# Optimization experiments

Hardware: AMD Instinct MI355X
Metric: run time of the kernel (lower is better)

## Reference

```python
import jax, jax.numpy as jnp
import numpy as np

N_NODES = 100000
N_EDGES = 1600000
IN_DIM = 128      # 1 (degree) + 127 (raw feat)
HID = 128
N_GRAPHS = 100


def setup_inputs() -> dict:
    key = jax.random.key(0)
    ks = jax.random.split(key, 16)
    feat = jax.random.normal(ks[0], (N_NODES, IN_DIM - 1), dtype=jnp.float32)
    src = jax.random.randint(ks[1], (N_EDGES,), 0, N_NODES, dtype=jnp.int32)
    dst = jax.random.randint(ks[2], (N_EDGES,), 0, N_NODES, dtype=jnp.int32)
    graph_ids = jnp.sort(jax.random.randint(ks[3], (N_NODES,), 0, N_GRAPHS, dtype=jnp.int32))
    s = 1.0 / np.sqrt(IN_DIM)
    W0 = jax.random.uniform(ks[4], (HID, IN_DIM), jnp.float32, -s, s)
    b0 = jax.random.uniform(ks[5], (HID,), jnp.float32, -s, s)
    s = 1.0 / np.sqrt(HID)
    W1 = jax.random.uniform(ks[6], (HID, HID), jnp.float32, -s, s)
    b1 = jax.random.uniform(ks[7], (HID,), jnp.float32, -s, s)
    W2 = jax.random.uniform(ks[8], (HID, HID), jnp.float32, -s, s)
    b2 = jax.random.uniform(ks[9], (HID,), jnp.float32, -s, s)
    Wc1 = jax.random.uniform(ks[10], (HID, HID), jnp.float32, -s, s)
    bc1 = jax.random.uniform(ks[11], (HID,), jnp.float32, -s, s)
    Wc2 = jax.random.uniform(ks[12], (1, HID), jnp.float32, -s, s)
    bc2 = jax.random.uniform(ks[13], (1,), jnp.float32, -s, s)
    return {"feat": feat, "src": src, "dst": dst, "graph_ids": graph_ids,
            "num_graphs": N_GRAPHS,
            "W0": W0, "b0": b0, "W1": W1, "b1": b1, "W2": W2, "b2": b2,
            "Wc1": Wc1, "bc1": bc1, "Wc2": Wc2, "bc2": bc2}


def _gcn_layer(h, src, dst, deg, W, b):
    # mean over in-neighbor messages; zero-in-degree nodes keep old h (DGL reduce never fires)
    n = h.shape[0]
    summed = jax.ops.segment_sum(h[src], dst, num_segments=n)  # [N, d]
    mean = summed / jnp.maximum(deg, 1.0)[:, None]
    agg = jnp.where((deg > 0)[:, None], mean, h)
    return jax.nn.relu(agg @ W.T + b)


def reference(feat, src, dst, graph_ids, num_graphs,
              W0, b0, W1, b1, W2, b2, Wc1, bc1, Wc2, bc2):
    n = feat.shape[0]
    deg = jax.ops.segment_sum(jnp.ones(src.shape[0], jnp.float32), dst, num_segments=n)  # in-degrees
    h = jnp.concatenate([deg[:, None], feat], axis=-1)  # [N, IN_DIM]
    for W, b in ((W0, b0), (W1, b1), (W2, b2)):
        h = _gcn_layer(h, src, dst, deg, W, b)
    # dgl.mean_nodes: per-graph mean of node features
    counts = jax.ops.segment_sum(jnp.ones(n, jnp.float32), graph_ids, num_segments=num_graphs)
    hg = jax.ops.segment_sum(h, graph_ids, num_segments=num_graphs) / jnp.maximum(counts, 1.0)[:, None]
    # faithful: classify1 applied twice, no activation (F.relu was passed as bias flag)
    hg = hg @ Wc1.T + bc1
    hg = hg @ Wc1.T + bc1
    hg = hg @ Wc2.T + bc2
    return hg  # [num_graphs, 1]
```

## Files before the change

### kernel.cpp

```cpp
#include <hip/hip_runtime.h>
#include <hip/hip_bf16.h>

#define HID 128
#define NRAW 127
#define BSH 8
#define BNODES 256


typedef __attribute__((ext_vector_type(8))) short short8;
typedef __attribute__((ext_vector_type(4))) float floatx4;
typedef __attribute__((ext_vector_type(2))) float floatx2;

__device__ inline unsigned pack_bf2(float x, float y) {
    unsigned bx = __float_as_uint(x);
    unsigned by = __float_as_uint(y);
    bx += 0x7fffu + ((bx >> 16) & 1u);
    by += 0x7fffu + ((by >> 16) & 1u);
    return (bx >> 16) | (by & 0xffff0000u);
}
__device__ inline float bf_lo(unsigned u) { return __uint_as_float(u << 16); }
__device__ inline float bf_hi(unsigned u) { return __uint_as_float(u & 0xffff0000u); }


__global__ void init_kernel(const float* __restrict__ W0, const float* __restrict__ W1,
                            const float* __restrict__ W2, const float* __restrict__ Wc1,
                            unsigned* __restrict__ O0, unsigned* __restrict__ O1,
                            unsigned* __restrict__ O2, float* __restrict__ Wc1p,
                            int* __restrict__ gbucket, float* __restrict__ hg,
                            float* __restrict__ counts,
                            unsigned* __restrict__ h8a, unsigned* __restrict__ h8b,
                            int G, int N) {
    int id = blockIdx.x * blockDim.x + threadIdx.x;
    if (id < 512) gbucket[id] = 0;
    if (id < G * HID) hg[id] = 0.f;
    if (id < G) counts[id] = 0.f;
    if (id < 32) {
        h8a[(size_t)N * 32 + id] = 0u;
        h8b[(size_t)N * 32 + id] = 0u;
    }
    if (id < 16384) {
        int t = id >> 7, p = id & 127;
        Wc1p[id] = Wc1[t * 128 + ((p & 7) * 16 + (p >> 3))];
    }
    if (id < 3 * 8192) {
        int sel = id >> 13, l = id & 8191;
        const float* W = sel == 0 ? W0 : (sel == 1 ? W1 : W2);
        unsigned* O = sel == 0 ? O0 : (sel == 1 ? O1 : O2);
        int o = l >> 6, pp = (l & 63) * 2;
        int k0 = (pp & 7) * 16 + (pp >> 3);
        int k1 = ((pp + 1) & 7) * 16 + ((pp + 1) >> 3);
        O[l] = pack_bf2(W[o * 128 + k0], W[o * 128 + k1]);
    }
}


__global__ __launch_bounds__(256) void bucket_count_kernel(const int* __restrict__ dst,
                                                           int* __restrict__ gbucket,
                                                           int E, int NB) {
    __shared__ int hist[512];
    int t = threadIdx.x;
    for (int b = t; b < NB; b += 256) hist[b] = 0;
    __syncthreads();
    int base = blockIdx.x * 4096;
    #pragma unroll
    for (int j = 0; j < 16; ++j) {
        int e = base + j * 256 + t;
        if (e < E) atomicAdd(&hist[dst[e] >> BSH], 1);
    }
    __syncthreads();
    for (int b = t; b < NB; b += 256) {
        int v = hist[b];
        if (v) atomicAdd(&gbucket[b], v);
    }
}

__global__ void bucket_scan_kernel(const int* __restrict__ gbucket, int* __restrict__ bstart,
                                   int* __restrict__ gcur, int NB, int E) {
    __shared__ int sm[512];
    int t = threadIdx.x;
    int v = (t < NB) ? gbucket[t] : 0;
    sm[t] = v;
    __syncthreads();
    for (int off = 1; off < 512; off <<= 1) {
        int add = (t >= off) ? sm[t - off] : 0;
        __syncthreads();
        sm[t] += add;
        __syncthreads();
    }
    if (t < NB) {
        int ex = sm[t] - v;
        bstart[t] = ex;
        gcur[t] = ex;
    }
    if (t == 0) bstart[NB] = E;
}

__global__ __launch_bounds__(256) void bucket_scatter_kernel(const int* __restrict__ src,
                                                             const int* __restrict__ dst,
                                                             int* __restrict__ gcur,
                                                             unsigned* __restrict__ staging,
                                                             int E, int NB) {
    __shared__ int hist[512];
    __shared__ int base[512];
    int t = threadIdx.x;
    for (int b = t; b < NB; b += 256) hist[b] = 0;
    __syncthreads();
    int s[16], d[16], r[16];
    int e0 = blockIdx.x * 4096;
    #pragma unroll
    for (int j = 0; j < 16; ++j) {
        int e = e0 + j * 256 + t;
        if (e < E) {
            s[j] = src[e];
            d[j] = dst[e];
            r[j] = atomicAdd(&hist[d[j] >> BSH], 1);
        } else d[j] = -1;
    }
    __syncthreads();
    for (int b = t; b < NB; b += 256) {
        int v = hist[b];
        base[b] = v ? atomicAdd(&gcur[b], v) : 0;
    }
    __syncthreads();
    #pragma unroll
    for (int j = 0; j < 16; ++j) {
        if (d[j] >= 0) {
            int b = d[j] >> BSH;
            staging[base[b] + r[j]] = ((unsigned)s[j] << 8) | ((unsigned)d[j] & 255u);
        }
    }
}

__global__ __launch_bounds__(256) void csr_build_kernel(const unsigned* __restrict__ staging,
                                                        const int* __restrict__ bstart,
                                                        int* __restrict__ rp, int* __restrict__ csr,
                                                        float* __restrict__ degf,
                                                        int N, int E, int NB) {
    __shared__ int hist[256];
    __shared__ int sm[256];
    __shared__ int excl[256];
    __shared__ int cnt[256];
    int t = threadIdx.x;
    int b = blockIdx.x;
    int nbase = b << BSH;
    int s0 = bstart[b], e1 = bstart[b + 1];
    hist[t] = 0;
    __syncthreads();
    for (int i = s0 + t; i < e1; i += 256) {
        unsigned p = staging[i];
        atomicAdd(&hist[p & (BNODES - 1)], 1);
    }
    __syncthreads();
    int h = hist[t];
    sm[t] = h;
    __syncthreads();
    for (int off = 1; off < 256; off <<= 1) {
        int add = (t >= off) ? sm[t - off] : 0;
        __syncthreads();
        sm[t] += add;
        __syncthreads();
    }
    excl[t] = sm[t] - h;
    cnt[t] = 0;
    int n = nbase + t;
    if (n < N) {
        rp[n] = s0 + (sm[t] - h);
        degf[n] = (float)h;
    }
    if (b == NB - 1 && t == 0) {
        rp[N] = E;
        degf[N] = 0.f;
    }
    __syncthreads();
    for (int i = s0 + t; i < e1; i += 256) {
        unsigned p = staging[i];
        int dl = p & (BNODES - 1);
        int pos = s0 + excl[dl] + atomicAdd(&cnt[dl], 1);
        csr[pos] = (int)(p >> 8);
    }
}


__global__ __launch_bounds__(256) void build_h0_kernel(const float* __restrict__ feat,
                                                       unsigned* __restrict__ h8, int N) {
    __shared__ float lf[8 * NRAW];
    int t = threadIdx.x;
    int n0 = blockIdx.x * 8;
    int nrows = min(8, N - n0);
    int total = nrows * NRAW;
    for (int j = t; j < total; j += 256) lf[j] = feat[(size_t)n0 * NRAW + j];
    __syncthreads();
    int n = t >> 5, c = t & 31;
    if (n < nrows) {
        const float* fr = lf + n * NRAW;
        int base = c >> 1, hb = (c & 1) * 4;
        float f[4];
        #pragma unroll
        for (int j = 0; j < 4; ++j) {
            int l = (hb + j) * 16 + base;
            f[j] = (l == 0) ? 0.f : fr[l - 1];
        }
        unsigned w = __builtin_amdgcn_cvt_pk_fp8_f32(f[0], f[1], 0, false);
        w = __builtin_amdgcn_cvt_pk_fp8_f32(f[2], f[3], w, true);
        h8[(size_t)(n0 + n) * 32 + c] = w;
    }
}


__global__ __launch_bounds__(256) void gcn_fused_kernel(const unsigned* __restrict__ h8,
                                                        unsigned* __restrict__ out8,
                                                        unsigned* __restrict__ outb,
                                                        const unsigned* __restrict__ Wb,
                                                        const float* __restrict__ bias,
                                                        const int* __restrict__ rp,
                                                        const int* __restrict__ csr,
                                                        const float* __restrict__ degf,
                                                        int col0fix, int N) {
    __shared__ unsigned Al[16 * 64];
    __shared__ unsigned Cs[16 * 64];
    int t = threadIdx.x;
    int wv = t >> 6, lane = t & 63;
    int s = lane >> 4;
    int c = lane & 15;
    int n0 = blockIdx.x * 16;
    const char* hbase = (const char*)h8;
    unsigned cOff = (unsigned)c * 8u;

    for (int nn = 0; nn < 4; ++nn) {
        int g = wv * 4 + nn;
        int i = n0 + g;
        if (i >= N) break;
        int start = rp[i], end = rp[i + 1];
        int deg = end - start;
        floatx2 a0 = {0.f, 0.f}, a1 = {0.f, 0.f}, a2 = {0.f, 0.f}, a3 = {0.f, 0.f};
        float dsum = 0.f;

        if (deg > 0) {
            int q = start + s;
            int idx = N;
            if (q < end) idx = csr[q];
            for (int p = start; p < end; p += 4) {
                uint2 v = *(const uint2*)(hbase + (((unsigned)idx << 7) + cOff));
                float dg = 0.f;
                if (col0fix && c == 0) dg = degf[idx];
                int q2 = p + 4 + s;
                int idxN = N;
                if (q2 < end) idxN = csr[q2];
                a0 += __builtin_amdgcn_cvt_pk_f32_fp8(v.x, false);
                a1 += __builtin_amdgcn_cvt_pk_f32_fp8(v.x, true);
                a2 += __builtin_amdgcn_cvt_pk_f32_fp8(v.y, false);
                a3 += __builtin_amdgcn_cvt_pk_f32_fp8(v.y, true);
                if (col0fix && c == 0) dsum += dg;
                idx = idxN;
            }
            a0[0] += __shfl_xor(a0[0], 16); a0[1] += __shfl_xor(a0[1], 16);
            a1[0] += __shfl_xor(a1[0], 16); a1[1] += __shfl_xor(a1[1], 16);
            a2[0] += __shfl_xor(a2[0], 16); a2[1] += __shfl_xor(a2[1], 16);
            a3[0] += __shfl_xor(a3[0], 16); a3[1] += __shfl_xor(a3[1], 16);
            a0[0] += __shfl_xor(a0[0], 32); a0[1] += __shfl_xor(a0[1], 32);
            a1[0] += __shfl_xor(a1[0], 32); a1[1] += __shfl_xor(a1[1], 32);
            a2[0] += __shfl_xor(a2[0], 32); a2[1] += __shfl_xor(a2[1], 32);
            a3[0] += __shfl_xor(a3[0], 32); a3[1] += __shfl_xor(a3[1], 32);
            if (col0fix) {
                dsum += __shfl_xor(dsum, 16);
                dsum += __shfl_xor(dsum, 32);
            }
        }

        float f0, f1, f2, f3, f4, f5, f6, f7;
        if (deg > 0) {
            if (col0fix && c == 0) a0[0] = dsum;
            float inv = 1.f / (float)deg;
            f0 = a0[0] * inv; f1 = a0[1] * inv;
            f2 = a1[0] * inv; f3 = a1[1] * inv;
            f4 = a2[0] * inv; f5 = a2[1] * inv;
            f6 = a3[0] * inv; f7 = a3[1] * inv;
        } else {
            uint2 v = *(const uint2*)(hbase + (((unsigned)i << 7) + cOff));
            floatx2 l0 = __builtin_amdgcn_cvt_pk_f32_fp8(v.x, false);
            floatx2 h0 = __builtin_amdgcn_cvt_pk_f32_fp8(v.x, true);
            floatx2 l1 = __builtin_amdgcn_cvt_pk_f32_fp8(v.y, false);
            floatx2 h1 = __builtin_amdgcn_cvt_pk_f32_fp8(v.y, true);
            f0 = l0[0]; f1 = l0[1]; f2 = h0[0]; f3 = h0[1];
            f4 = l1[0]; f5 = l1[1]; f6 = h1[0]; f7 = h1[1];
        }
        if (s == 0) {
            uint4 r;
            r.x = pack_bf2(f0, f1);
            r.y = pack_bf2(f2, f3);
            r.z = pack_bf2(f4, f5);
            r.w = pack_bf2(f6, f7);
            *(uint4*)&Al[(g * 16 + (c ^ (g & 7))) * 4] = r;
        }
    }
    __syncthreads();

    {
        int m = lane & 15, q = lane >> 4;
        floatx4 acc0 = (floatx4)(0.f), acc1 = (floatx4)(0.f);
        #pragma unroll
        for (int kt = 0; kt < 4; ++kt) {
            short8 af = *(const short8*)&Al[(m * 16 + ((kt * 4 + q) ^ (m & 7))) * 4];
            short8 b0 = *(const short8*)&Wb[((2 * wv) * 16 + m) * 64 + kt * 16 + q * 4];
            short8 b1 = *(const short8*)&Wb[((2 * wv + 1) * 16 + m) * 64 + kt * 16 + q * 4];
            acc0 = __builtin_amdgcn_mfma_f32_16x16x32_bf16(af, b0, acc0, 0, 0, 0);
            acc1 = __builtin_amdgcn_mfma_f32_16x16x32_bf16(af, b1, acc1, 0, 0, 0);
        }
        float bv0 = bias[(2 * wv) * 16 + m];
        float bv1 = bias[(2 * wv + 1) * 16 + m];
        #pragma unroll
        for (int r4 = 0; r4 < 4; ++r4) {
            int row = q * 4 + r4;
            float v0 = fmaxf(acc0[r4] + bv0, 0.f);
            float v1 = fmaxf(acc1[r4] + bv1, 0.f);
            if (out8) {
                unsigned pk = __builtin_amdgcn_cvt_pk_fp8_f32(v0, v1, 0, false);
                *(unsigned short*)((char*)Cs + row * 128 + m * 8 + 2 * wv) = (unsigned short)pk;
            } else {
                Cs[row * 64 + m * 4 + wv] = pack_bf2(v0, v1);
            }
        }
    }
    __syncthreads();

    {
        int row = t >> 4, cc = t & 15;
        int n = n0 + row;
        if (n < N) {
            if (out8)
                ((uint2*)out8)[(size_t)n * 16 + cc] =
                    *(const uint2*)((const char*)Cs + row * 128 + cc * 8);
            else
                ((uint4*)outb)[(size_t)n * 16 + cc] = *(const uint4*)&Cs[row * 64 + cc * 4];
        }
    }
}


__global__ __launch_bounds__(256) void pool_kernel(const unsigned* __restrict__ h,
                                                   const int* __restrict__ gid,
                                                   float* __restrict__ hg,
                                                   float* __restrict__ counts, int N) {
    int c = threadIdx.x & 63;
    int q = threadIdx.x >> 6;
    int n0 = blockIdx.x * 64;
    int nend = min(n0 + 64, N);
    float ax = 0.f, ay = 0.f, cnt = 0.f;
    int cur = -1;
    for (int n = n0 + q; n < nend; n += 4) {
        int g = gid[n];
        if (g != cur) {
            if (cur >= 0) {
                atomicAdd(&hg[cur * HID + 2 * c], ax);
                atomicAdd(&hg[cur * HID + 2 * c + 1], ay);
                if (c == 0) atomicAdd(&counts[cur], cnt);
            }
            ax = ay = cnt = 0.f;
            cur = g;
        }
        unsigned v = h[(size_t)n * 64 + c];
        ax += bf_lo(v); ay += bf_hi(v);
        cnt += 1.f;
    }
    if (cur >= 0) {
        atomicAdd(&hg[cur * HID + 2 * c], ax);
        atomicAdd(&hg[cur * HID + 2 * c + 1], ay);
        if (c == 0) atomicAdd(&counts[cur], cnt);
    }
}


__global__ __launch_bounds__(128) void cls_fused_kernel(const float* __restrict__ hg,
                                                        const float* __restrict__ counts,
                                                        const float* __restrict__ Wc1p,
                                                        const float* __restrict__ Wc1,
                                                        const float* __restrict__ bc1,
                                                        const float* __restrict__ Wc2,
                                                        const float* __restrict__ bc2,
                                                        float* __restrict__ out, int G) {
    __shared__ float x[128];
    __shared__ float y[128];
    __shared__ float red[128];
    int g = blockIdx.x, t = threadIdx.x;
    float inv = 1.f / fmaxf(counts[g], 1.f);
    x[t] = hg[g * HID + t] * inv;
    __syncthreads();
    const float4* wp4 = (const float4*)(Wc1p + t * HID);
    float s = 0.f;
    #pragma unroll
    for (int k4 = 0; k4 < 32; ++k4) {
        float4 w = wp4[k4];
        s += x[k4 * 4] * w.x + x[k4 * 4 + 1] * w.y + x[k4 * 4 + 2] * w.z + x[k4 * 4 + 3] * w.w;
    }
    y[t] = s + bc1[t];
    __syncthreads();
    const float4* w4 = (const float4*)(Wc1 + t * HID);
    float s2 = 0.f;
    #pragma unroll
    for (int k4 = 0; k4 < 32; ++k4) {
        float4 w = w4[k4];
        s2 += y[k4 * 4] * w.x + y[k4 * 4 + 1] * w.y + y[k4 * 4 + 2] * w.z + y[k4 * 4 + 3] * w.w;
    }
    red[t] = (s2 + bc1[t]) * Wc2[t];
    __syncthreads();
    if (t < 64) {
        float r = red[t] + red[t + 64];
        #pragma unroll
        for (int off = 32; off > 0; off >>= 1) r += __shfl_down(r, off);
        if (t == 0) out[g] = r + bc2[0];
    }
}


extern "C" void kernel_launch(void* const* d_in, const int* in_sizes, int n_in,
                              void* d_out, int out_size, void* d_ws, size_t ws_size,
                              hipStream_t stream) {
    const float* feat = (const float*)d_in[0];
    const int* src    = (const int*)d_in[1];
    const int* dst    = (const int*)d_in[2];
    const int* gid    = (const int*)d_in[3];
    const float* W0  = (const float*)d_in[5];
    const float* b0  = (const float*)d_in[6];
    const float* W1  = (const float*)d_in[7];
    const float* b1  = (const float*)d_in[8];
    const float* W2  = (const float*)d_in[9];
    const float* b2  = (const float*)d_in[10];
    const float* Wc1 = (const float*)d_in[11];
    const float* bc1 = (const float*)d_in[12];
    const float* Wc2 = (const float*)d_in[13];
    const float* bc2 = (const float*)d_in[14];

    const int N = in_sizes[3];
    const int E = in_sizes[1];
    const int G = out_size;
    const int NB = (N + BNODES - 1) >> BSH;

    char* ws = (char*)d_ws;
    size_t off = 0;
    auto alloc = [&](size_t bytes) { void* p = ws + off; off += (bytes + 255) & ~size_t(255); return p; };
    unsigned* h8a    = (unsigned*)alloc((size_t)(N + 1) * 32 * 4);
    unsigned* h8b    = (unsigned*)alloc((size_t)(N + 1) * 32 * 4);
    unsigned* hB     = (unsigned*)alloc((size_t)N * 64 * 4);
    float* degf      = (float*)alloc((size_t)(N + 1) * 4);
    unsigned* staging = (unsigned*)alloc((size_t)E * 4);
    int* csr         = (int*)alloc((size_t)(E + 64) * 4);
    int* rp          = (int*)alloc((size_t)(N + 1) * 4);
    int* gbucket     = (int*)alloc(512 * 4);
    int* bstart      = (int*)alloc(513 * 4);
    int* gcur        = (int*)alloc(512 * 4);
    unsigned* Wb0    = (unsigned*)alloc(8192 * 4);
    unsigned* Wb1    = (unsigned*)alloc(8192 * 4);
    unsigned* Wb2    = (unsigned*)alloc(8192 * 4);
    float* Wc1p      = (float*)alloc(16384 * 4);
    float* hg        = (float*)alloc((size_t)G * HID * 4);
    float* counts    = (float*)alloc((size_t)G * 4);

    init_kernel<<<96, 256, 0, stream>>>(W0, W1, W2, Wc1, Wb0, Wb1, Wb2, Wc1p,
                                        gbucket, hg, counts, h8a, h8b, G, N);

    int gE = (E + 4095) / 4096;
    bucket_count_kernel<<<gE, 256, 0, stream>>>(dst, gbucket, E, NB);
    bucket_scan_kernel<<<1, 512, 0, stream>>>(gbucket, bstart, gcur, NB, E);
    bucket_scatter_kernel<<<gE, 256, 0, stream>>>(src, dst, gcur, staging, E, NB);
    csr_build_kernel<<<NB, 256, 0, stream>>>(staging, bstart, rp, csr, degf, N, E, NB);

    build_h0_kernel<<<(N + 7) / 8, 256, 0, stream>>>(feat, h8a, N);

    int layer_grid = (N + 15) / 16;
    gcn_fused_kernel<<<layer_grid, 256, 0, stream>>>(h8a, h8b, nullptr, Wb0, b0, rp, csr, degf, 1, N);
    gcn_fused_kernel<<<layer_grid, 256, 0, stream>>>(h8b, h8a, nullptr, Wb1, b1, rp, csr, degf, 0, N);
    gcn_fused_kernel<<<layer_grid, 256, 0, stream>>>(h8a, nullptr, hB, Wb2, b2, rp, csr, degf, 0, N);

    pool_kernel<<<(N + 63) / 64, 256, 0, stream>>>(hB, gid, hg, counts, N);

    cls_fused_kernel<<<G, 128, 0, stream>>>(hg, counts, Wc1p, Wc1, bc1, Wc2, bc2,
                                            (float*)d_out, G);
}
```

Baseline: 421.8 us.

## Restructure GCN gather: 8 lanes per node, staged CSR indices in LDS, 32-node tiles

```diff
diff --git a/kernel.cpp b/kernel.cpp
--- a/kernel.cpp
+++ b/kernel.cpp
@@ -5,6 +5,7 @@
 #define NRAW 127
 #define BSH 8
 #define BNODES 256
+#define EW 2048
 
 
 typedef __attribute__((ext_vector_type(8))) short short8;
@@ -207,133 +208,160 @@
 }
 
 
-__global__ __launch_bounds__(256) void gcn_fused_kernel(const unsigned* __restrict__ h8,
-                                                        unsigned* __restrict__ out8,
-                                                        unsigned* __restrict__ outb,
-                                                        const unsigned* __restrict__ Wb,
-                                                        const float* __restrict__ bias,
-                                                        const int* __restrict__ rp,
-                                                        const int* __restrict__ csr,
-                                                        const float* __restrict__ degf,
-                                                        int col0fix, int N) {
-    __shared__ unsigned Al[16 * 64];
-    __shared__ unsigned Cs[16 * 64];
+__global__ __launch_bounds__(256, 4) void gcn_fused_kernel(const unsigned* __restrict__ h8,
+                                                           unsigned* __restrict__ out8,
+                                                           unsigned* __restrict__ outb,
+                                                           const unsigned* __restrict__ Wb,
+                                                           const float* __restrict__ bias,
+                                                           const int* __restrict__ rp,
+                                                           const int* __restrict__ csr,
+                                                           const float* __restrict__ degf,
+                                                           int col0fix, int N) {
+    __shared__ unsigned Al[32 * 64];
+    __shared__ unsigned CsS[32 * 64];
+    int* sIdx = (int*)CsS;
     int t = threadIdx.x;
     int wv = t >> 6, lane = t & 63;
-    int s = lane >> 4;
-    int c = lane & 15;
-    int n0 = blockIdx.x * 16;
+    int grp = lane >> 3;
+    int cc4 = lane & 7;
+    int n0 = blockIdx.x * 32;
+    int g32 = wv * 8 + grp;
+    int i = n0 + g32;
     const char* hbase = (const char*)h8;
-    unsigned cOff = (unsigned)c * 8u;
-
-    for (int nn = 0; nn < 4; ++nn) {
-        int g = wv * 4 + nn;
-        int i = n0 + g;
-        if (i >= N) break;
-        int start = rp[i], end = rp[i + 1];
-        int deg = end - start;
-        floatx2 a0 = {0.f, 0.f}, a1 = {0.f, 0.f}, a2 = {0.f, 0.f}, a3 = {0.f, 0.f};
-        float dsum = 0.f;
-
-        if (deg > 0) {
-            int q = start + s;
-            int idx = N;
-            if (q < end) idx = csr[q];
-            for (int p = start; p < end; p += 4) {
-                uint2 v = *(const uint2*)(hbase + (((unsigned)idx << 7) + cOff));
-                float dg = 0.f;
-                if (col0fix && c == 0) dg = degf[idx];
-                int q2 = p + 4 + s;
-                int idxN = N;
-                if (q2 < end) idxN = csr[q2];
-                a0 += __builtin_amdgcn_cvt_pk_f32_fp8(v.x, false);
-                a1 += __builtin_amdgcn_cvt_pk_f32_fp8(v.x, true);
-                a2 += __builtin_amdgcn_cvt_pk_f32_fp8(v.y, false);
-                a3 += __builtin_amdgcn_cvt_pk_f32_fp8(v.y, true);
-                if (col0fix && c == 0) dsum += dg;
-                idx = idxN;
-            }
-            a0[0] += __shfl_xor(a0[0], 16); a0[1] += __shfl_xor(a0[1], 16);
-            a1[0] += __shfl_xor(a1[0], 16); a1[1] += __shfl_xor(a1[1], 16);
-            a2[0] += __shfl_xor(a2[0], 16); a2[1] += __shfl_xor(a2[1], 16);
-            a3[0] += __shfl_xor(a3[0], 16); a3[1] += __shfl_xor(a3[1], 16);
-            a0[0] += __shfl_xor(a0[0], 32); a0[1] += __shfl_xor(a0[1], 32);
-            a1[0] += __shfl_xor(a1[0], 32); a1[1] += __shfl_xor(a1[1], 32);
-            a2[0] += __shfl_xor(a2[0], 32); a2[1] += __shfl_xor(a2[1], 32);
-            a3[0] += __shfl_xor(a3[0], 32); a3[1] += __shfl_xor(a3[1], 32);
-            if (col0fix) {
-                dsum += __shfl_xor(dsum, 16);
-                dsum += __shfl_xor(dsum, 32);
-            }
-        }
-
-        float f0, f1, f2, f3, f4, f5, f6, f7;
-        if (deg > 0) {
-            if (col0fix && c == 0) a0[0] = dsum;
-            float inv = 1.f / (float)deg;
-            f0 = a0[0] * inv; f1 = a0[1] * inv;
-            f2 = a1[0] * inv; f3 = a1[1] * inv;
-            f4 = a2[0] * inv; f5 = a2[1] * inv;
-            f6 = a3[0] * inv; f7 = a3[1] * inv;
+    unsigned c16 = (unsigned)cc4 * 16u;
+
+    int start = 0, end = 0;
+    if (i < N) { start = rp[i]; end = rp[i + 1]; }
+    int deg = end - start;
+    int nEnd = min(n0 + 32, N);
+    int s0 = rp[n0];
+    int e1 = rp[nEnd];
+
+    floatx2 a0 = {0.f, 0.f}, a1 = {0.f, 0.f}, a2 = {0.f, 0.f}, a3 = {0.f, 0.f};
+    floatx2 a4 = {0.f, 0.f}, a5 = {0.f, 0.f}, a6 = {0.f, 0.f}, a7 = {0.f, 0.f};
+    float dsum = 0.f;
+
+    #define GATH4(ii) (*(const uint4*)(hbase + (((unsigned)(ii) << 7) + c16)))
+    #define ACC4(vv) do { \
+        a0 += __builtin_amdgcn_cvt_pk_f32_fp8((vv).x, false); \
+        a1 += __builtin_amdgcn_cvt_pk_f32_fp8((vv).x, true);  \
+        a2 += __builtin_amdgcn_cvt_pk_f32_fp8((vv).y, false); \
+        a3 += __builtin_amdgcn_cvt_pk_f32_fp8((vv).y, true);  \
+        a4 += __builtin_amdgcn_cvt_pk_f32_fp8((vv).z, false); \
+        a5 += __builtin_amdgcn_cvt_pk_f32_fp8((vv).z, true);  \
+        a6 += __builtin_amdgcn_cvt_pk_f32_fp8((vv).w, false); \
+        a7 += __builtin_amdgcn_cvt_pk_f32_fp8((vv).w, true);  \
+    } while (0)
+
+    for (int w0 = s0; w0 < e1; w0 += EW) {
+        if (w0 > s0) __syncthreads();
+        int wcnt = min(EW, e1 - w0);
+        for (int j = t; j < wcnt; j += 256) sIdx[j] = csr[w0 + j];
+        __syncthreads();
+        int p  = max(start, w0) - w0;
+        int pe = min(end, w0 + wcnt) - w0;
+        for (; p + 4 <= pe; p += 4) {
+            int iA = sIdx[p], iB = sIdx[p + 1], iC = sIdx[p + 2], iD = sIdx[p + 3];
+            uint4 vA = GATH4(iA), vB = GATH4(iB), vC = GATH4(iC), vD = GATH4(iD);
+            if (col0fix && cc4 == 0)
+                dsum += degf[iA] + degf[iB] + degf[iC] + degf[iD];
+            ACC4(vA); ACC4(vB); ACC4(vC); ACC4(vD);
+        }
+        for (; p + 2 <= pe; p += 2) {
+            int iA = sIdx[p], iB = sIdx[p + 1];
+            uint4 vA = GATH4(iA), vB = GATH4(iB);
+            if (col0fix && cc4 == 0) dsum += degf[iA] + degf[iB];
+            ACC4(vA); ACC4(vB);
+        }
+        for (; p < pe; ++p) {
+            int iA = sIdx[p];
+            uint4 vA = GATH4(iA);
+            if (col0fix && cc4 == 0) dsum += degf[iA];
+            ACC4(vA);
+        }
+    }
+
+    if (i < N) {
+        float inv;
+        if (deg == 0) {
+            uint4 v = GATH4(i);
+            ACC4(v);
+            inv = 1.f;
         } else {
-            uint2 v = *(const uint2*)(hbase + (((unsigned)i << 7) + cOff));
-            floatx2 l0 = __builtin_amdgcn_cvt_pk_f32_fp8(v.x, false);
-            floatx2 h0 = __builtin_amdgcn_cvt_pk_f32_fp8(v.x, true);
-            floatx2 l1 = __builtin_amdgcn_cvt_pk_f32_fp8(v.y, false);
-            floatx2 h1 = __builtin_amdgcn_cvt_pk_f32_fp8(v.y, true);
-            f0 = l0[0]; f1 = l0[1]; f2 = h0[0]; f3 = h0[1];
-            f4 = l1[0]; f5 = l1[1]; f6 = h1[0]; f7 = h1[1];
-        }
-        if (s == 0) {
-            uint4 r;
-            r.x = pack_bf2(f0, f1);
-            r.y = pack_bf2(f2, f3);
-            r.z = pack_bf2(f4, f5);
-            r.w = pack_bf2(f6, f7);
-            *(uint4*)&Al[(g * 16 + (c ^ (g & 7))) * 4] = r;
-        }
+            if (col0fix && cc4 == 0) a0[0] = dsum;
+            inv = 1.f / (float)deg;
+        }
+        uint4 r0, r1;
+        r0.x = pack_bf2(a0[0] * inv, a0[1] * inv);
+        r0.y = pack_bf2(a1[0] * inv, a1[1] * inv);
+        r0.z = pack_bf2(a2[0] * inv, a2[1] * inv);
+        r0.w = pack_bf2(a3[0] * inv, a3[1] * inv);
+        r1.x = pack_bf2(a4[0] * inv, a4[1] * inv);
+        r1.y = pack_bf2(a5[0] * inv, a5[1] * inv);
+        r1.z = pack_bf2(a6[0] * inv, a6[1] * inv);
+        r1.w = pack_bf2(a7[0] * inv, a7[1] * inv);
+        int gr0 = 2 * cc4, gr1 = 2 * cc4 + 1;
+        *(uint4*)&Al[(g32 * 16 + (gr0 ^ (g32 & 7))) * 4] = r0;
+        *(uint4*)&Al[(g32 * 16 + (gr1 ^ (g32 & 7))) * 4] = r1;
     }
     __syncthreads();
 
     {
+        int rh = wv & 1, cq = wv >> 1;
         int m = lane & 15, q = lane >> 4;
+        int r = rh * 16 + m;
         floatx4 acc0 = (floatx4)(0.f), acc1 = (floatx4)(0.f);
+        floatx4 acc2 = (floatx4)(0.f), acc3 = (floatx4)(0.f);
         #pragma unroll
         for (int kt = 0; kt < 4; ++kt) {
-            short8 af = *(const short8*)&Al[(m * 16 + ((kt * 4 + q) ^ (m & 7))) * 4];
-            short8 b0 = *(const short8*)&Wb[((2 * wv) * 16 + m) * 64 + kt * 16 + q * 4];
-            short8 b1 = *(const short8*)&Wb[((2 * wv + 1) * 16 + m) * 64 + kt * 16 + q * 4];
+            short8 af = *(const short8*)&Al[(r * 16 + ((kt * 4 + q) ^ (m & 7))) * 4];
+            short8 b0 = *(const short8*)&Wb[((cq * 4 + 0) * 16 + m) * 64 + kt * 16 + q * 4];
+            short8 b1 = *(const short8*)&Wb[((cq * 4 + 1) * 16 + m) * 64 + kt * 16 + q * 4];
+            short8 b2 = *(const short8*)&Wb[((cq * 4 + 2) * 16 + m) * 64 + kt * 16 + q * 4];
+            short8 b3 = *(const short8*)&Wb[((cq * 4 + 3) * 16 + m) * 64 + kt * 16 + q * 4];
             acc0 = __builtin_amdgcn_mfma_f32_16x16x32_bf16(af, b0, acc0, 0, 0, 0);
             acc1 = __builtin_amdgcn_mfma_f32_16x16x32_bf16(af, b1, acc1, 0, 0, 0);
-        }
-        float bv0 = bias[(2 * wv) * 16 + m];
-        float bv1 = bias[(2 * wv + 1) * 16 + m];
+            acc2 = __builtin_amdgcn_mfma_f32_16x16x32_bf16(af, b2, acc2, 0, 0, 0);
+            acc3 = __builtin_amdgcn_mfma_f32_16x16x32_bf16(af, b3, acc3, 0, 0, 0);
+        }
+        float bv0 = bias[(cq * 4 + 0) * 16 + m];
+        float bv1 = bias[(cq * 4 + 1) * 16 + m];
+        float bv2 = bias[(cq * 4 + 2) * 16 + m];
+        float bv3 = bias[(cq * 4 + 3) * 16 + m];
         #pragma unroll
         for (int r4 = 0; r4 < 4; ++r4) {
-            int row = q * 4 + r4;
+            int row = rh * 16 + q * 4 + r4;
             float v0 = fmaxf(acc0[r4] + bv0, 0.f);
             float v1 = fmaxf(acc1[r4] + bv1, 0.f);
+            float v2 = fmaxf(acc2[r4] + bv2, 0.f);
+            float v3 = fmaxf(acc3[r4] + bv3, 0.f);
             if (out8) {
                 unsigned pk = __builtin_amdgcn_cvt_pk_fp8_f32(v0, v1, 0, false);
-                *(unsigned short*)((char*)Cs + row * 128 + m * 8 + 2 * wv) = (unsigned short)pk;
+                pk = __builtin_amdgcn_cvt_pk_fp8_f32(v2, v3, pk, true);
+                *(unsigned*)((char*)CsS + row * 128 + m * 8 + cq * 4) = pk;
             } else {
-                Cs[row * 64 + m * 4 + wv] = pack_bf2(v0, v1);
+                CsS[row * 64 + m * 4 + cq * 2 + 0] = pack_bf2(v0, v1);
+                CsS[row * 64 + m * 4 + cq * 2 + 1] = pack_bf2(v2, v3);
             }
         }
     }
     __syncthreads();
 
     {
-        int row = t >> 4, cc = t & 15;
+        int row = t >> 3, gg = t & 7;
         int n = n0 + row;
         if (n < N) {
-            if (out8)
-                ((uint2*)out8)[(size_t)n * 16 + cc] =
-                    *(const uint2*)((const char*)Cs + row * 128 + cc * 8);
-            else
-                ((uint4*)outb)[(size_t)n * 16 + cc] = *(const uint4*)&Cs[row * 64 + cc * 4];
-        }
-    }
+            if (out8) {
+                ((uint4*)out8)[(size_t)n * 8 + gg] =
+                    *(const uint4*)((const char*)CsS + row * 128 + gg * 16);
+            } else {
+                ((uint4*)outb)[(size_t)n * 16 + 2 * gg]     = *(const uint4*)&CsS[row * 64 + 8 * gg];
+                ((uint4*)outb)[(size_t)n * 16 + 2 * gg + 1] = *(const uint4*)&CsS[row * 64 + 8 * gg + 4];
+            }
+        }
+    }
+    #undef GATH4
+    #undef ACC4
 }
 
 
@@ -466,7 +494,7 @@
 
     build_h0_kernel<<<(N + 7) / 8, 256, 0, stream>>>(feat, h8a, N);
 
-    int layer_grid = (N + 15) / 16;
+    int layer_grid = (N + 31) / 32;
     gcn_fused_kernel<<<layer_grid, 256, 0, stream>>>(h8a, h8b, nullptr, Wb0, b0, rp, csr, degf, 1, N);
     gcn_fused_kernel<<<layer_grid, 256, 0, stream>>>(h8b, h8a, nullptr, Wb1, b1, rp, csr, degf, 0, N);
     gcn_fused_kernel<<<layer_grid, 256, 0, stream>>>(h8a, nullptr, hB, Wb2, b2, rp, csr, degf, 0, N);
```

Result: faster. 356.0 us (-15.6%).
